# Optimization experiments

Measured on AMD Instinct MI355X. Metric: run time of the kernel, lower is better.

The kernel has to match this reference:

```python
import jax, jax.numpy as jnp
import numpy as np

B, S, D = 2, 2048, 1024
H = 16
HD = D // H  # 64
FORESIGHT = -1e9  # masked_fill value for non-causal positions


def setup_inputs() -> dict:
    key = jax.random.key(0)
    ks = jax.random.split(key, 8)
    s = 0.02
    return {
        "x": jax.random.normal(ks[0], (B, S, D), dtype=jnp.float32),
        "Wq": jax.random.normal(ks[1], (D, H * HD), dtype=jnp.float32) * s,
        "bq": jax.random.normal(ks[2], (H * HD,), dtype=jnp.float32) * s,
        "Wk": jax.random.normal(ks[3], (D, H * HD), dtype=jnp.float32) * s,
        "Wv": jax.random.normal(ks[4], (D, H * HD), dtype=jnp.float32) * s,
        "Wo": jax.random.normal(ks[5], (H * HD, D), dtype=jnp.float32) * s,
        "bo": jax.random.normal(ks[6], (D,), dtype=jnp.float32) * s,
    }


def reference(x, Wq, bq, Wk, Wv, Wo, bo):
    b, s, _ = x.shape
    # projections -> [B, H, S, HD]
    q = (x @ Wq + bq).reshape(b, s, H, HD).transpose(0, 2, 1, 3)
    k = (x @ Wk).reshape(b, s, H, HD).transpose(0, 2, 1, 3)
    v = (x @ Wv).reshape(b, s, H, HD).transpose(0, 2, 1, 3)
    # scores [B, H, S, S]
    scores = jnp.einsum("bhqd,bhkd->bhqk", q, k) / jnp.sqrt(jnp.float32(HD))
    # ALiBi bias: slope_h * j (key position), broadcast over queries
    slopes = 2.0 ** (-8.0 * jnp.arange(1, H + 1, dtype=jnp.float32) / H)
    positions = jnp.arange(s, dtype=jnp.float32)
    scores = scores - slopes[None, :, None, None] * positions[None, None, None, :]
    # causal mask: fill strictly-upper triangle with foresight
    causal = jnp.tril(jnp.ones((s, s), dtype=bool))
    scores = jnp.where(causal[None, None, :, :], scores, FORESIGHT)
    attn = jax.nn.softmax(scores, axis=-1)
    out = jnp.einsum("bhqk,bhkd->bhqd", attn, v)
    out = out.transpose(0, 2, 1, 3).reshape(b, s, H * HD)
    return out @ Wo + bo
```

## Files before the change

### kernel.cpp

```cpp
#include <hip/hip_runtime.h>
#include <stdint.h>

#define DDIM 1024
#define HH 16
#define HDIM 64
#define SS 2048

typedef short bf16x8 __attribute__((ext_vector_type(8)));
typedef short bf16x4 __attribute__((ext_vector_type(4)));
typedef float f32x4 __attribute__((ext_vector_type(4)));
typedef unsigned short u16;

__device__ __forceinline__ unsigned f2bf(float f) {
  unsigned u = __builtin_bit_cast(unsigned, f);
  u = u + 0x7FFFu + ((u >> 16) & 1u);
  return u >> 16;
}

__device__ __forceinline__ unsigned cvt_pk_bf16(float a, float b) {
  unsigned r;
  asm("v_cvt_pk_bf16_f32 %0, %1, %2" : "=v"(r) : "v"(a), "v"(b));
  return r;
}

__device__ __forceinline__ void mfma16(f32x4& c, bf16x4 a, bf16x4 b) {
  asm("v_mfma_f32_16x16x16_bf16 %0, %1, %2, %0" : "+v"(c) : "v"(a), "v"(b));
}

__device__ __forceinline__ void gload16(const void* g, void* l) {
  __builtin_amdgcn_global_load_lds(
      (const __attribute__((address_space(1))) unsigned int*)g,
      (__attribute__((address_space(3))) unsigned int*)l, 16, 0, 0);
}

__global__ void k_convert_x(const float* __restrict__ x, u16* __restrict__ xb) {
  int i = (blockIdx.x * 256 + threadIdx.x) * 4;
  float4 v = *(const float4*)(x + i);
  ushort4 o;
  o.x = (u16)f2bf(v.x); o.y = (u16)f2bf(v.y); o.z = (u16)f2bf(v.z); o.w = (u16)f2bf(v.w);
  *(ushort4*)(xb + i) = o;
}

__global__ void k_transpose_w(const float* __restrict__ w0, const float* __restrict__ w1,
                              const float* __restrict__ w2, const float* __restrict__ w3,
                              u16* __restrict__ wt) {
  __shared__ float t[64][65];
  int z = blockIdx.z;
  const float* src = (z == 0) ? w0 : (z == 1) ? w1 : (z == 2) ? w2 : w3;
  u16* dst = wt + (size_t)z * DDIM * DDIM;
  int k0 = blockIdx.x * 64, n0 = blockIdx.y * 64;
  int tid = threadIdx.x;
  int c4 = tid & 15, rr = tid >> 4;
  for (int rep = 0; rep < 4; rep++) {
    int r = rr + rep * 16;
    float4 v = *(const float4*)(src + (size_t)(k0 + r) * DDIM + n0 + c4 * 4);
    t[r][c4 * 4 + 0] = v.x; t[r][c4 * 4 + 1] = v.y;
    t[r][c4 * 4 + 2] = v.z; t[r][c4 * 4 + 3] = v.w;
  }
  __syncthreads();
  for (int rep = 0; rep < 4; rep++) {
    int n = rr + rep * 16;
    ushort4 o;
    o.x = (u16)f2bf(t[c4 * 4 + 0][n]); o.y = (u16)f2bf(t[c4 * 4 + 1][n]);
    o.z = (u16)f2bf(t[c4 * 4 + 2][n]); o.w = (u16)f2bf(t[c4 * 4 + 3][n]);
    *(ushort4*)(dst + (size_t)(n0 + n) * DDIM + k0 + c4 * 4) = o;
  }
}

template <int MODE>
__global__ __launch_bounds__(256, 2) void k_gemm(const u16* __restrict__ A,
                                                 const u16* __restrict__ BT,
                                                 const float* __restrict__ bias,
                                                 void* __restrict__ O0,
                                                 void* __restrict__ O1,
                                                 void* __restrict__ O2) {
  __shared__ __align__(16) u16 lA[128 * 64];
  __shared__ __align__(16) u16 lB[128 * 64];
  const int tid = threadIdx.x;
  const int l = tid & 63, w = tid >> 6;
  const int wm = w >> 1, wn = w & 1;
  const int m0 = blockIdx.x * 128, n0 = blockIdx.y * 128;
  const int lr = l >> 4, lc = l & 15;

  const int srow = l >> 3;
  const int scol = ((l & 7) ^ srow) * 8;

  f32x4 acc[4][4];
  for (int mi = 0; mi < 4; mi++)
    for (int ni = 0; ni < 4; ni++)
      acc[mi][ni] = f32x4{0.f, 0.f, 0.f, 0.f};

  for (int kk = 0; kk < 16; kk++) {
    const int k0 = kk * 64;
    for (int i = 0; i < 4; i++) {
      int c = w * 4 + i;
      gload16(A + (size_t)(m0 + c * 8 + srow) * DDIM + k0 + scol, (char*)lA + c * 1024);
      gload16(BT + (size_t)(n0 + c * 8 + srow) * DDIM + k0 + scol, (char*)lB + c * 1024);
    }
    __syncthreads();
    for (int ks = 0; ks < 2; ks++) {
      bf16x8 af[4], bfr[4];
      for (int mi = 0; mi < 4; mi++) {
        int row = wm * 64 + mi * 16 + lc;
        int slot = (ks * 4 + lr) ^ (row & 7);
        af[mi] = *(const bf16x8*)((const char*)lA + row * 128 + slot * 16);
      }
      for (int ni = 0; ni < 4; ni++) {
        int row = wn * 64 + ni * 16 + lc;
        int slot = (ks * 4 + lr) ^ (row & 7);
        bfr[ni] = *(const bf16x8*)((const char*)lB + row * 128 + slot * 16);
      }
      for (int mi = 0; mi < 4; mi++)
        for (int ni = 0; ni < 4; ni++)
          acc[mi][ni] = __builtin_amdgcn_mfma_f32_16x16x32_bf16(af[mi], bfr[ni], acc[mi][ni], 0, 0, 0);
    }
    __syncthreads();
  }

  if (MODE == 0) {
    const int which = blockIdx.y >> 3;
    if (which == 0) {
      u16* C = (u16*)O0;
      const float c1 = 0.18033688011112043f;
      for (int mi = 0; mi < 4; mi++)
        for (int ni = 0; ni < 4; ni++) {
          int nl = (n0 + wn * 64 + ni * 16 + lc) & 1023;
          float badd = bias[nl];
          for (int r = 0; r < 4; r++) {
            int m = m0 + wm * 64 + mi * 16 + lr * 4 + r;
            C[(size_t)m * DDIM + nl] = (u16)f2bf((acc[mi][ni][r] + badd) * c1);
          }
        }
    } else if (which == 1) {
      u16* C = (u16*)O1;
      for (int mi = 0; mi < 4; mi++)
        for (int ni = 0; ni < 4; ni++) {
          int nl = (n0 + wn * 64 + ni * 16 + lc) & 1023;
          for (int r = 0; r < 4; r++) {
            int m = m0 + wm * 64 + mi * 16 + lr * 4 + r;
            C[(size_t)m * DDIM + nl] = (u16)f2bf(acc[mi][ni][r]);
          }
        }
    } else {
      u16* C = (u16*)O2;
      for (int mi = 0; mi < 4; mi++)
        for (int ni = 0; ni < 4; ni++) {
          int nl = (n0 + wn * 64 + ni * 16 + lc) & 1023;
          int h = nl >> 6, hd = nl & 63;
          int m = m0 + wm * 64 + mi * 16 + lr * 4;
          int b = m >> 11, s = m & 2047;
          unsigned d0 = f2bf(acc[mi][ni][0]) | (f2bf(acc[mi][ni][1]) << 16);
          unsigned d1 = f2bf(acc[mi][ni][2]) | (f2bf(acc[mi][ni][3]) << 16);
          u16* p = C + ((size_t)((b * HH + h) * HDIM + hd)) * SS + s;
          *(unsigned*)(p) = d0;
          *(unsigned*)(p + 2) = d1;
        }
    }
  } else {
    float* C = (float*)O0;
    for (int mi = 0; mi < 4; mi++)
      for (int ni = 0; ni < 4; ni++) {
        int n = n0 + wn * 64 + ni * 16 + lc;
        float badd = bias[n];
        for (int r = 0; r < 4; r++) {
          int m = m0 + wm * 64 + mi * 16 + lr * 4 + r;
          C[(size_t)m * DDIM + n] = acc[mi][ni][r] + badd;
        }
      }
  }
}

__device__ __forceinline__ void attn_tile(int kt, bool masked, int kfhi,
                                          const char* lKc, const char* lVc,
                                          const bf16x8 qf[2], f32x4 of[4],
                                          float& mrun, float& lrun,
                                          float slope2, int lr, int lc, int q_glob) {
  f32x4 sf[8];
#pragma unroll
  for (int kf = 0; kf < 8; kf++) sf[kf] = f32x4{0.f, 0.f, 0.f, 0.f};
  __builtin_amdgcn_s_setprio(1);
#pragma unroll
  for (int ks = 0; ks < 2; ks++)
#pragma unroll
    for (int kf = 0; kf < 8; kf++) {
      if (kf >= kfhi) continue;
      int key = kf * 16 + lc;
      int slot = (ks * 4 + lr) ^ (lc & 7);
      bf16x8 a = *(const bf16x8*)(lKc + key * 128 + slot * 16);
      sf[kf] = __builtin_amdgcn_mfma_f32_16x16x32_bf16(a, qf[ks], sf[kf], 0, 0, 0);
    }
  __builtin_amdgcn_s_setprio(0);

  const float kbase = -slope2 * (float)(kt * 128 + lr * 4);
  float tmax = -3.0e38f;
#pragma unroll
  for (int kf = 0; kf < 8; kf++) {
    if (kf >= kfhi) continue;
#pragma unroll
    for (int r = 0; r < 4; r++) {
      float sv = sf[kf][r] + (kbase - slope2 * (float)(kf * 16 + r));
      if (masked) {
        int key = kt * 128 + kf * 16 + lr * 4 + r;
        if (key > q_glob) sv = -3.0e38f;
      }
      sf[kf][r] = sv;
      tmax = fmaxf(tmax, sv);
    }
  }
  tmax = fmaxf(tmax, __shfl_xor(tmax, 16));
  tmax = fmaxf(tmax, __shfl_xor(tmax, 32));

  if (tmax > mrun) {
    float corr = exp2f(mrun - tmax);
    lrun *= corr;
#pragma unroll
    for (int mf = 0; mf < 4; mf++) {
      of[mf][0] *= corr; of[mf][1] *= corr; of[mf][2] *= corr; of[mf][3] *= corr;
    }
    mrun = tmax;
  }

  f32x4 ps = f32x4{0.f, 0.f, 0.f, 0.f};
  bf16x4 pb[8];
#pragma unroll
  for (int kf = 0; kf < 8; kf++) {
    if (kf >= kfhi) continue;
    float p0 = exp2f(sf[kf][0] - mrun);
    float p1 = exp2f(sf[kf][1] - mrun);
    float p2 = exp2f(sf[kf][2] - mrun);
    float p3 = exp2f(sf[kf][3] - mrun);
    ps[0] += p0; ps[1] += p1; ps[2] += p2; ps[3] += p3;
    uint2 uu;
    uu.x = cvt_pk_bf16(p0, p1);
    uu.y = cvt_pk_bf16(p2, p3);
    pb[kf] = __builtin_bit_cast(bf16x4, uu);
  }
  float psum = (ps[0] + ps[1]) + (ps[2] + ps[3]);
  psum += __shfl_xor(psum, 16);
  psum += __shfl_xor(psum, 32);
  lrun += psum;

  __builtin_amdgcn_s_setprio(1);
#pragma unroll
  for (int kf = 0; kf < 8; kf++) {
    if (kf >= kfhi) continue;
    int g2 = (kf << 1) + (lr >> 1);
#pragma unroll
    for (int mf = 0; mf < 4; mf++) {
      int hd = mf * 16 + lc;
      int byte = hd * 256 + ((g2 ^ (hd & 7)) << 4) + ((lr & 1) << 3);
      bf16x4 va = *(const bf16x4*)(lVc + byte);
      mfma16(of[mf], va, pb[kf]);
    }
  }
  __builtin_amdgcn_s_setprio(0);
}

__global__ __launch_bounds__(256, 4) void k_attn(const u16* __restrict__ Q,
                                                 const u16* __restrict__ Kg,
                                                 const u16* __restrict__ Vt,
                                                 u16* __restrict__ AO) {
  __shared__ __align__(16) u16 lK[128 * 64];
  __shared__ __align__(16) u16 lV[64 * 128];

  const int tid = threadIdx.x;
  const int l = tid & 63, w = tid >> 6;
  const int lr = l >> 4, lc = l & 15;
  const int id = blockIdx.x;
  const int bh = id >> 5;
  const int p5 = id & 31;
  const int kq = p5 >> 1;
  const int qt = (p5 & 1) ? (31 - kq) : kq;
  const int b = bh >> 4, h = bh & 15;

  const float slope2 = exp2f(-0.5f * (float)(h + 1)) * 1.4426950408889634f;
  const int q_glob = qt * 64 + w * 16 + lc;

  bf16x8 qf[2];
#pragma unroll
  for (int ks = 0; ks < 2; ks++)
    qf[ks] = *(const bf16x8*)(Q + (size_t)(b * SS + q_glob) * DDIM + h * HDIM + ks * 32 + lr * 8);

  f32x4 of[4];
#pragma unroll
  for (int mf = 0; mf < 4; mf++) of[mf] = f32x4{0.f, 0.f, 0.f, 0.f};
  float mrun = -3.0e38f, lrun = 0.f;

  const int srowK = l >> 3;
  const int scolK = ((l & 7) ^ srowK) * 8;
  const int nkt = qt / 2 + 1;

  auto stage = [&](int kt) {
#pragma unroll
    for (int i = 0; i < 4; i++) {
      int c = w * 4 + i;
      gload16(Kg + (size_t)(b * SS + kt * 128 + c * 8 + srowK) * DDIM + h * HDIM + scolK,
              (char*)lK + c * 1024);
      int hd = c * 4 + lr;
      gload16(Vt + ((size_t)bh * HDIM + hd) * SS + kt * 128 + (((l & 15) ^ (hd & 7)) << 3),
              (char*)lV + c * 1024);
    }
  };

  for (int kt = 0; kt < nkt - 1; kt++) {
    stage(kt);
    __syncthreads();
    attn_tile(kt, false, 8, (const char*)lK, (const char*)lV, qf, of, mrun, lrun,
              slope2, lr, lc, q_glob);
    __syncthreads();
  }
  stage(nkt - 1);
  __syncthreads();
  if (qt & 1)
    attn_tile(nkt - 1, true, 8, (const char*)lK, (const char*)lV, qf, of, mrun, lrun,
              slope2, lr, lc, q_glob);
  else
    attn_tile(nkt - 1, true, 4, (const char*)lK, (const char*)lV, qf, of, mrun, lrun,
              slope2, lr, lc, q_glob);

  float inv = 1.f / lrun;
  u16* obase = AO + (size_t)(b * SS + q_glob) * DDIM + h * HDIM;
#pragma unroll
  for (int mf = 0; mf < 4; mf++) {
    uint2 uu;
    uu.x = cvt_pk_bf16(of[mf][0] * inv, of[mf][1] * inv);
    uu.y = cvt_pk_bf16(of[mf][2] * inv, of[mf][3] * inv);
    *(uint2*)(obase + mf * 16 + lr * 4) = uu;
  }
}

extern "C" void kernel_launch(void* const* d_in, const int* in_sizes, int n_in,
                              void* d_out, int out_size, void* d_ws, size_t ws_size,
                              hipStream_t stream) {
  const float* x  = (const float*)d_in[0];
  const float* Wq = (const float*)d_in[1];
  const float* bq = (const float*)d_in[2];
  const float* Wk = (const float*)d_in[3];
  const float* Wv = (const float*)d_in[4];
  const float* Wo = (const float*)d_in[5];
  const float* bo = (const float*)d_in[6];
  float* out = (float*)d_out;

  u16* ws = (u16*)d_ws;
  const size_t MEG = 1024 * 1024;
  u16* xb = ws;
  u16* WT = ws + 4 * MEG;
  u16* Qb = ws + 8 * MEG;
  u16* Kb = ws + 12 * MEG;
  u16* Vt = ws + 16 * MEG;
  u16* AO = ws + 20 * MEG;

  k_convert_x<<<dim3(4096), dim3(256), 0, stream>>>(x, xb);
  k_transpose_w<<<dim3(16, 16, 4), dim3(256), 0, stream>>>(Wq, Wk, Wv, Wo, WT);
  k_gemm<0><<<dim3(32, 24), dim3(256), 0, stream>>>(xb, WT, bq, (void*)Qb, (void*)Kb, (void*)Vt);
  k_attn<<<dim3(1024), dim3(256), 0, stream>>>(Qb, Kb, Vt, AO);
  k_gemm<1><<<dim3(32, 8), dim3(256), 0, stream>>>(AO, WT + 3 * MEG, bo, (void*)out, nullptr, nullptr);
}
```

Baseline: 141.7 us.

## Double-buffer K/V tiles in attention and route P through LDS for 32-wide MFMA

Shrinks the attention key tile from 128 to 64 and double-buffers K and V in shared memory, so the next tile's global loads overlap compute on the current one. Each loop iteration now ends with one barrier instead of two. P is written to a per-wave LDS scratch and read back as bf16x8, so the PV product can use 16x16x32 MFMA instead of 16x16x16. The block ordering also changes so neighbouring blocks share a query tile across heads. The cost is extra LDS traffic for P, more iterations with more softmax rescale steps, and more LDS use per block, which may lower occupancy.

```diff
diff --git a/kernel.cpp b/kernel.cpp
--- a/kernel.cpp
+++ b/kernel.cpp
@@ -7,7 +7,6 @@
 #define SS 2048
 
 typedef short bf16x8 __attribute__((ext_vector_type(8)));
-typedef short bf16x4 __attribute__((ext_vector_type(4)));
 typedef float f32x4 __attribute__((ext_vector_type(4)));
 typedef unsigned short u16;
 
@@ -21,10 +20,6 @@
   unsigned r;
   asm("v_cvt_pk_bf16_f32 %0, %1, %2" : "=v"(r) : "v"(a), "v"(b));
   return r;
-}
-
-__device__ __forceinline__ void mfma16(f32x4& c, bf16x4 a, bf16x4 b) {
-  asm("v_mfma_f32_16x16x16_bf16 %0, %1, %2, %0" : "+v"(c) : "v"(a), "v"(b));
 }
 
 __device__ __forceinline__ void gload16(const void* g, void* l) {
@@ -170,20 +165,19 @@
   }
 }
 
-__device__ __forceinline__ void attn_tile(int kt, bool masked, int kfhi,
-                                          const char* lKc, const char* lVc,
+__device__ __forceinline__ void attn_tile(int kt, bool masked,
+                                          const char* lKc, const char* lVc, char* lPw,
                                           const bf16x8 qf[2], f32x4 of[4],
                                           float& mrun, float& lrun,
                                           float slope2, int lr, int lc, int q_glob) {
-  f32x4 sf[8];
-#pragma unroll
-  for (int kf = 0; kf < 8; kf++) sf[kf] = f32x4{0.f, 0.f, 0.f, 0.f};
+  f32x4 sf[4];
+#pragma unroll
+  for (int kf = 0; kf < 4; kf++) sf[kf] = f32x4{0.f, 0.f, 0.f, 0.f};
   __builtin_amdgcn_s_setprio(1);
 #pragma unroll
   for (int ks = 0; ks < 2; ks++)
 #pragma unroll
-    for (int kf = 0; kf < 8; kf++) {
-      if (kf >= kfhi) continue;
+    for (int kf = 0; kf < 4; kf++) {
       int key = kf * 16 + lc;
       int slot = (ks * 4 + lr) ^ (lc & 7);
       bf16x8 a = *(const bf16x8*)(lKc + key * 128 + slot * 16);
@@ -191,22 +185,20 @@
     }
   __builtin_amdgcn_s_setprio(0);
 
-  const float kbase = -slope2 * (float)(kt * 128 + lr * 4);
+  const float base = -slope2 * (float)(kt * 64 + lr * 4);
   float tmax = -3.0e38f;
 #pragma unroll
-  for (int kf = 0; kf < 8; kf++) {
-    if (kf >= kfhi) continue;
+  for (int kf = 0; kf < 4; kf++)
 #pragma unroll
     for (int r = 0; r < 4; r++) {
-      float sv = sf[kf][r] + (kbase - slope2 * (float)(kf * 16 + r));
+      float sv = sf[kf][r] + (base - slope2 * (float)(kf * 16 + r));
       if (masked) {
-        int key = kt * 128 + kf * 16 + lr * 4 + r;
+        int key = kt * 64 + kf * 16 + lr * 4 + r;
         if (key > q_glob) sv = -3.0e38f;
       }
       sf[kf][r] = sv;
       tmax = fmaxf(tmax, sv);
     }
-  }
   tmax = fmaxf(tmax, __shfl_xor(tmax, 16));
   tmax = fmaxf(tmax, __shfl_xor(tmax, 32));
 
@@ -221,10 +213,8 @@
   }
 
   f32x4 ps = f32x4{0.f, 0.f, 0.f, 0.f};
-  bf16x4 pb[8];
-#pragma unroll
-  for (int kf = 0; kf < 8; kf++) {
-    if (kf >= kfhi) continue;
+#pragma unroll
+  for (int kf = 0; kf < 4; kf++) {
     float p0 = exp2f(sf[kf][0] - mrun);
     float p1 = exp2f(sf[kf][1] - mrun);
     float p2 = exp2f(sf[kf][2] - mrun);
@@ -233,7 +223,8 @@
     uint2 uu;
     uu.x = cvt_pk_bf16(p0, p1);
     uu.y = cvt_pk_bf16(p2, p3);
-    pb[kf] = __builtin_bit_cast(bf16x4, uu);
+    int slot = ((kf * 2 + (lr >> 1)) ^ (lc & 7));
+    *(uint2*)(lPw + lc * 128 + slot * 16 + (lr & 1) * 8) = uu;
   }
   float psum = (ps[0] + ps[1]) + (ps[2] + ps[3]);
   psum += __shfl_xor(psum, 16);
@@ -242,15 +233,15 @@
 
   __builtin_amdgcn_s_setprio(1);
 #pragma unroll
-  for (int kf = 0; kf < 8; kf++) {
-    if (kf >= kfhi) continue;
-    int g2 = (kf << 1) + (lr >> 1);
+  for (int ks = 0; ks < 2; ks++) {
+    int slotp = (ks * 4 + lr) ^ (lc & 7);
+    bf16x8 pb = *(const bf16x8*)(lPw + lc * 128 + slotp * 16);
 #pragma unroll
     for (int mf = 0; mf < 4; mf++) {
       int hd = mf * 16 + lc;
-      int byte = hd * 256 + ((g2 ^ (hd & 7)) << 4) + ((lr & 1) << 3);
-      bf16x4 va = *(const bf16x4*)(lVc + byte);
-      mfma16(of[mf], va, pb[kf]);
+      int slotv = (ks * 4 + lr) ^ (lc & 7);
+      bf16x8 va = *(const bf16x8*)(lVc + hd * 128 + slotv * 16);
+      of[mf] = __builtin_amdgcn_mfma_f32_16x16x32_bf16(va, pb, of[mf], 0, 0, 0);
     }
   }
   __builtin_amdgcn_s_setprio(0);
@@ -260,17 +251,18 @@
                                                  const u16* __restrict__ Kg,
                                                  const u16* __restrict__ Vt,
                                                  u16* __restrict__ AO) {
-  __shared__ __align__(16) u16 lK[128 * 64];
-  __shared__ __align__(16) u16 lV[64 * 128];
+  __shared__ __align__(16) u16 lK[2][64 * 64];
+  __shared__ __align__(16) u16 lV[2][64 * 64];
+  __shared__ __align__(16) u16 lP[4][16 * 64];
 
   const int tid = threadIdx.x;
   const int l = tid & 63, w = tid >> 6;
   const int lr = l >> 4, lc = l & 15;
   const int id = blockIdx.x;
-  const int bh = id >> 5;
-  const int p5 = id & 31;
-  const int kq = p5 >> 1;
-  const int qt = (p5 & 1) ? (31 - kq) : kq;
+  const int bh = id & 31;
+  const int s5 = (id >> 5) & 1;
+  const int gg = id >> 6;
+  const int qt = s5 ? (31 - gg) : gg;
   const int b = bh >> 4, h = bh & 15;
 
   const float slope2 = exp2f(-0.5f * (float)(h + 1)) * 1.4426950408889634f;
@@ -286,37 +278,39 @@
   for (int mf = 0; mf < 4; mf++) of[mf] = f32x4{0.f, 0.f, 0.f, 0.f};
   float mrun = -3.0e38f, lrun = 0.f;
 
-  const int srowK = l >> 3;
-  const int scolK = ((l & 7) ^ srowK) * 8;
-  const int nkt = qt / 2 + 1;
-
-  auto stage = [&](int kt) {
-#pragma unroll
-    for (int i = 0; i < 4; i++) {
-      int c = w * 4 + i;
-      gload16(Kg + (size_t)(b * SS + kt * 128 + c * 8 + srowK) * DDIM + h * HDIM + scolK,
-              (char*)lK + c * 1024);
-      int hd = c * 4 + lr;
-      gload16(Vt + ((size_t)bh * HDIM + hd) * SS + kt * 128 + (((l & 15) ^ (hd & 7)) << 3),
-              (char*)lV + c * 1024);
+  const int srow = l >> 3;
+  const int scol = ((l & 7) ^ srow) * 8;
+  const int nkt = qt + 1;
+  char* lPw = (char*)lP[w];
+
+  auto stage = [&](int kt, int bb) {
+#pragma unroll
+    for (int i = 0; i < 2; i++) {
+      int c = i * 4 + w;
+      gload16(Kg + (size_t)(b * SS + kt * 64 + c * 8 + srow) * DDIM + h * HDIM + scol,
+              (char*)lK[bb] + c * 1024);
+      gload16(Vt + ((size_t)bh * HDIM + c * 8 + srow) * SS + kt * 64 + scol,
+              (char*)lV[bb] + c * 1024);
     }
   };
 
+  stage(0, 0);
+  asm volatile("s_waitcnt vmcnt(0)" ::: "memory");
+  __builtin_amdgcn_s_barrier();
+  asm volatile("" ::: "memory");
+
   for (int kt = 0; kt < nkt - 1; kt++) {
-    stage(kt);
-    __syncthreads();
-    attn_tile(kt, false, 8, (const char*)lK, (const char*)lV, qf, of, mrun, lrun,
-              slope2, lr, lc, q_glob);
-    __syncthreads();
-  }
-  stage(nkt - 1);
-  __syncthreads();
-  if (qt & 1)
-    attn_tile(nkt - 1, true, 8, (const char*)lK, (const char*)lV, qf, of, mrun, lrun,
-              slope2, lr, lc, q_glob);
-  else
-    attn_tile(nkt - 1, true, 4, (const char*)lK, (const char*)lV, qf, of, mrun, lrun,
-              slope2, lr, lc, q_glob);
+    const int cur = kt & 1;
+    stage(kt + 1, cur ^ 1);
+    attn_tile(kt, false, (const char*)lK[cur], (const char*)lV[cur], lPw,
+              qf, of, mrun, lrun, slope2, lr, lc, q_glob);
+    asm volatile("s_waitcnt vmcnt(0)" ::: "memory");
+    __builtin_amdgcn_s_barrier();
+    asm volatile("" ::: "memory");
+  }
+  const int cur = (nkt - 1) & 1;
+  attn_tile(nkt - 1, true, (const char*)lK[cur], (const char*)lV[cur], lPw,
+            qf, of, mrun, lrun, slope2, lr, lc, q_glob);
 
   float inv = 1.f / lrun;
   u16* obase = AO + (size_t)(b * SS + q_glob) * DDIM + h * HDIM;
```

Result: faster. 124.5 us (-12.2%).
